# Kernel optimization log

Hardware: AMD Instinct MI355X
Metric: run time of the kernel (lower is better)

## Reference

```python
import jax, jax.numpy as jnp
import numpy as np

N = 10000          # nodes
E = 80000          # edges
STATE_DIM = 18
HID = 1024
LAYERS = 4


def setup_inputs() -> dict:
    key = jax.random.key(0)
    ks = jax.random.split(key, 16)
    s = 0.02
    x = jax.random.normal(ks[0], (N, STATE_DIM), dtype=jnp.float32)
    edge_index = jax.random.randint(ks[1], (2, E), 0, N, dtype=jnp.int32)
    # frozen inverse-phase embedding projection (no bias)
    proj_w = jax.random.normal(ks[2], (STATE_DIM, HID), dtype=jnp.float32) * s
    # per-layer message MLP: Linear(2*HID -> HID) -> ReLU -> Linear(HID -> HID)
    W1 = jax.random.normal(ks[3], (LAYERS, 2 * HID, HID), dtype=jnp.float32) * s
    b1 = jnp.zeros((LAYERS, HID), dtype=jnp.float32)
    W2 = jax.random.normal(ks[4], (LAYERS, HID, HID), dtype=jnp.float32) * s
    b2 = jnp.zeros((LAYERS, HID), dtype=jnp.float32)
    # ghost head: Linear(HID->256) -> ReLU -> Linear(256->1) -> Sigmoid
    gw1 = jax.random.normal(ks[5], (HID, 256), dtype=jnp.float32) * s
    gb1 = jnp.zeros((256,), dtype=jnp.float32)
    gw2 = jax.random.normal(ks[6], (256, 1), dtype=jnp.float32) * s
    gb2 = jnp.zeros((1,), dtype=jnp.float32)
    # state head: Linear(HID -> STATE_DIM)
    sw = jax.random.normal(ks[7], (HID, STATE_DIM), dtype=jnp.float32) * s
    sb = jnp.zeros((STATE_DIM,), dtype=jnp.float32)
    return {"x": x, "edge_index": edge_index, "proj_w": proj_w,
            "W1": W1, "b1": b1, "W2": W2, "b2": b2,
            "gw1": gw1, "gb1": gb1, "gw2": gw2, "gb2": gb2,
            "sw": sw, "sb": sb}


def reference(x, edge_index, proj_w, W1, b1, W2, b2, gw1, gb1, gw2, gb2, sw, sb):
    src = edge_index[0]  # j (source)
    dst = edge_index[1]  # i (target), aggr='add' scatters into i
    # InversePhaseEmbedding: sin(h)*cos(h)
    p = x @ proj_w                      # [N, HID]
    h = jnp.sin(p) * jnp.cos(p)
    for l in range(LAYERS):
        x_i = h[dst]                    # [E, HID] gather target feats
        x_j = h[src]                    # [E, HID] gather source feats
        msg = jnp.concatenate([x_i, x_j - x_i], axis=-1)  # [E, 2*HID]
        m = jax.nn.relu(msg @ W1[l] + b1[l]) @ W2[l] + b2[l]  # [E, HID]
        h = jax.ops.segment_sum(m, dst, num_segments=N)       # scatter-add
        h = jax.nn.relu(h)
    ghost_score = jax.nn.sigmoid(jax.nn.relu(h @ gw1 + gb1) @ gw2 + gb2)  # [N,1]
    stable_state = h @ sw + sb                                            # [N,18]
    return ghost_score, stable_state, h
```

## Files before the change

kernel.cpp:

```cpp
#include <hip/hip_runtime.h>
#include <hip/hip_bf16.h>
#include <math.h>

#define NN 10000
#define EE 80000
#define SDIM 18
#define HID 1024
#define NLAYERS 4
#define GHID 256

typedef __bf16 bf16;
typedef __bf16 bf16x8 __attribute__((ext_vector_type(8)));
typedef __bf16 bf16x4 __attribute__((ext_vector_type(4)));
typedef float f32x4 __attribute__((ext_vector_type(4)));

#define AS1C(p) ((const __attribute__((address_space(1))) void*)(p))
#define AS3(p)  ((__attribute__((address_space(3))) void*)(p))

__global__ void count_kernel(const int* __restrict__ ei, int* __restrict__ cnt) {
    int e = blockIdx.x * 256 + threadIdx.x;
    if (e < EE) atomicAdd(&cnt[ei[EE + e]], 1);
}

__global__ __launch_bounds__(256) void scan_kernel(const int* __restrict__ cnt,
                                                   int* __restrict__ offs,
                                                   int* __restrict__ cursor,
                                                   float* __restrict__ degF) {
    const int CH = 40;
    __shared__ int partial[256];
    int t = threadIdx.x;
    int base = t * CH;
    int local[CH];
    int sum = 0;
#pragma unroll
    for (int i = 0; i < CH; ++i) {
        int idx = base + i;
        int v = (idx < NN) ? cnt[idx] : 0;
        local[i] = sum;
        sum += v;
    }
    partial[t] = sum;
    __syncthreads();
    for (int off = 1; off < 256; off <<= 1) {
        int v = (t >= off) ? partial[t - off] : 0;
        __syncthreads();
        partial[t] += v;
        __syncthreads();
    }
    int excl = (t == 0) ? 0 : partial[t - 1];
#pragma unroll
    for (int i = 0; i < CH; ++i) {
        int idx = base + i;
        if (idx < NN) {
            int o = excl + local[i];
            offs[idx] = o;
            cursor[idx] = o;
            degF[idx] = (float)cnt[idx];
        }
    }
    if (t == 255) offs[NN] = partial[255];
}

__global__ void scatter_kernel(const int* __restrict__ ei, int* __restrict__ cursor,
                               int* __restrict__ esrc) {
    int e = blockIdx.x * 256 + threadIdx.x;
    if (e < EE) {
        int dst = ei[EE + e];
        int pos = atomicAdd(&cursor[dst], 1);
        esrc[pos] = ei[e];
    }
}

__global__ __launch_bounds__(256) void prep_kernel(const float* __restrict__ W1,
                                                   const float* __restrict__ W2,
                                                   const float* __restrict__ gw1,
                                                   const float* __restrict__ sw,
                                                   const float* __restrict__ b1,
                                                   bf16* __restrict__ WT,
                                                   bf16* __restrict__ W2t,
                                                   bf16* __restrict__ gw1t,
                                                   bf16* __restrict__ swt,
                                                   float* __restrict__ cb,
                                                   int* __restrict__ cnt) {
    __shared__ float td[32][33];
    __shared__ float tb[32][33];
    const size_t H2 = (size_t)HID * HID;
    int b = blockIdx.x;
    int tx = threadIdx.x & 31, ty = threadIdx.x >> 5;

    if (b < 4096) {
        int l = b >> 10, r = b & 1023;
        int bx = (r & 31) * 32, by = (r >> 5) * 32;
        const float* s = W1 + (size_t)l * 2 * H2;
        bf16* d = WT + (size_t)l * 2 * H2;
#pragma unroll
        for (int r4 = 0; r4 < 4; ++r4) {
            int row = by + ty + r4 * 8;
            float vt = s[(size_t)row * HID + bx + tx];
            float vb = s[H2 + (size_t)row * HID + bx + tx];
            td[ty + r4 * 8][tx] = vt - vb;
            tb[ty + r4 * 8][tx] = vb;
        }
        __syncthreads();
#pragma unroll
        for (int r4 = 0; r4 < 4; ++r4) {
            int orow = bx + ty + r4 * 8;
            d[(size_t)orow * HID + by + tx] = (bf16)td[tx][ty + r4 * 8];
            d[(size_t)(HID + orow) * HID + by + tx] = (bf16)tb[tx][ty + r4 * 8];
        }
    } else if (b < 8192) {
        int sub = b - 4096;
        int l = sub >> 10, r = sub & 1023;
        int bx = (r & 31) * 32, by = (r >> 5) * 32;
        const float* s = W2 + (size_t)l * H2;
        bf16* d = W2t + (size_t)l * H2;
#pragma unroll
        for (int r4 = 0; r4 < 4; ++r4) {
            int row = by + ty + r4 * 8;
            td[ty + r4 * 8][tx] = s[(size_t)row * HID + bx + tx];
        }
        __syncthreads();
#pragma unroll
        for (int r4 = 0; r4 < 4; ++r4) {
            int orow = bx + ty + r4 * 8;
            d[(size_t)orow * HID + by + tx] = (bf16)td[tx][ty + r4 * 8];
        }
    } else if (b < 8448) {
        int sub = b - 8192;
        int bx = (sub & 7) * 32, by = (sub >> 3) * 32;
#pragma unroll
        for (int r4 = 0; r4 < 4; ++r4) {
            int row = by + ty + r4 * 8;
            td[ty + r4 * 8][tx] = gw1[(size_t)row * GHID + bx + tx];
        }
        __syncthreads();
#pragma unroll
        for (int r4 = 0; r4 < 4; ++r4) {
            int orow = bx + ty + r4 * 8;
            gw1t[(size_t)orow * HID + by + tx] = (bf16)td[tx][ty + r4 * 8];
        }
    } else if (b < 8576) {
        int i = (b - 8448) * 256 + threadIdx.x;
        int n = i >> 10, k = i & 1023;
        swt[i] = (bf16)(n < SDIM ? sw[k * SDIM + n] : 0.f);
    } else if (b < 8608) {
        int i = (b - 8576) * 256 + threadIdx.x;
        int l = i >> 11, c = i & 2047;
        cb[i] = (c < HID) ? b1[l * HID + c] : 0.f;
    } else {
        int i = (b - 8608) * 256 + threadIdx.x;
        if (i < NN) cnt[i] = 0;
    }
}

__global__ __launch_bounds__(256) void proj_kernel(const float* __restrict__ x,
                                                   const float* __restrict__ pw,
                                                   bf16* __restrict__ hb) {
    int row = blockIdx.y;
    int col = blockIdx.x * 256 + threadIdx.x;
    __shared__ float xr[SDIM];
    if (threadIdx.x < SDIM) xr[threadIdx.x] = x[row * SDIM + threadIdx.x];
    __syncthreads();
    float acc = 0.f;
#pragma unroll
    for (int k = 0; k < SDIM; ++k) acc += xr[k] * pw[k * HID + col];
    hb[(size_t)row * HID + col] = (bf16)(sinf(acc) * cosf(acc));
}

template <int RELU, int HAS_BIAS, int HAS_RS, int WF32, int WB16>
__global__ __launch_bounds__(256) void mgemm_kernel(const bf16* __restrict__ A,
                                                    const bf16* __restrict__ Bt,
                                                    float* __restrict__ C,
                                                    bf16* __restrict__ Cb,
                                                    const float* __restrict__ bias,
                                                    const float* __restrict__ rowscale,
                                                    int M, int N, int K) {
    __shared__ bf16 As[2][128 * 32];
    __shared__ bf16 Bs[2][128 * 32];
    const int tid = threadIdx.x;

    const int num_n = gridDim.x, num_m = gridDim.y;
    int bid = blockIdx.x + blockIdx.y * num_n;
    const int GROUP = 8;
    int width = GROUP * num_n;
    int group = bid / width;
    int rem = bid - group * width;
    int rows_ing = num_m - group * GROUP;
    rows_ing = rows_ing < GROUP ? rows_ing : GROUP;
    int by = group * GROUP + rem % rows_ing;
    int bx = rem / rows_ing;
    const int m0 = by * 128;
    const int n0 = bx * 128;

    const int wave = tid >> 6;
    const int wr = (wave >> 1) * 64, wc = (wave & 1) * 64;
    const int lane = tid & 63;
    const int quad = lane >> 4, r15 = lane & 15;

    f32x4 acc[4][4] = {};

    const int s0 = tid, s1 = 256 + tid;
    int ar0 = m0 + (s0 >> 2); ar0 = ar0 < M ? ar0 : M - 1;
    int ar1 = m0 + (s1 >> 2); ar1 = ar1 < M ? ar1 : M - 1;
    const bf16* ga0 = A + (size_t)ar0 * K + (s0 & 3) * 8;
    const bf16* ga1 = A + (size_t)ar1 * K + (s1 & 3) * 8;
    const bf16* gb0 = Bt + (size_t)(n0 + (s0 >> 2)) * K + (s0 & 3) * 8;
    const bf16* gb1 = Bt + (size_t)(n0 + (s1 >> 2)) * K + (s1 & 3) * 8;
    const int lofs0 = (tid & ~63) * 8;
    const int lofs1 = 2048 + (tid & ~63) * 8;

    __builtin_amdgcn_global_load_lds(AS1C(ga0), AS3(&As[0][lofs0]), 16, 0, 0);
    __builtin_amdgcn_global_load_lds(AS1C(ga1), AS3(&As[0][lofs1]), 16, 0, 0);
    __builtin_amdgcn_global_load_lds(AS1C(gb0), AS3(&Bs[0][lofs0]), 16, 0, 0);
    __builtin_amdgcn_global_load_lds(AS1C(gb1), AS3(&Bs[0][lofs1]), 16, 0, 0);

    const int NIT = K >> 5;
    for (int k = 0; k < NIT; ++k) {
        const int buf = k & 1;
        __syncthreads();
        if (k + 1 < NIT) {
            const int ko = (k + 1) << 5;
            __builtin_amdgcn_global_load_lds(AS1C(ga0 + ko), AS3(&As[buf ^ 1][lofs0]), 16, 0, 0);
            __builtin_amdgcn_global_load_lds(AS1C(ga1 + ko), AS3(&As[buf ^ 1][lofs1]), 16, 0, 0);
            __builtin_amdgcn_global_load_lds(AS1C(gb0 + ko), AS3(&Bs[buf ^ 1][lofs0]), 16, 0, 0);
            __builtin_amdgcn_global_load_lds(AS1C(gb1 + ko), AS3(&Bs[buf ^ 1][lofs1]), 16, 0, 0);
        }
        bf16x8 af[4], bfr[4];
#pragma unroll
        for (int i = 0; i < 4; ++i)
            af[i] = *(const bf16x8*)(&As[buf][(wr + i * 16 + r15) * 32 + quad * 8]);
#pragma unroll
        for (int j = 0; j < 4; ++j)
            bfr[j] = *(const bf16x8*)(&Bs[buf][(wc + j * 16 + r15) * 32 + quad * 8]);
#pragma unroll
        for (int i = 0; i < 4; ++i)
#pragma unroll
            for (int j = 0; j < 4; ++j)
                acc[i][j] = __builtin_amdgcn_mfma_f32_16x16x32_bf16(af[i], bfr[j], acc[i][j], 0, 0, 0);
    }

#pragma unroll
    for (int i = 0; i < 4; ++i) {
#pragma unroll
        for (int r = 0; r < 4; ++r) {
            int grow = m0 + wr + i * 16 + quad * 4 + r;
            if (grow >= M) continue;
            float rs = HAS_RS ? rowscale[grow] : 1.f;
#pragma unroll
            for (int j = 0; j < 4; ++j) {
                int gcol = n0 + wc + j * 16 + r15;
                float v = acc[i][j][r];
                if (HAS_BIAS) v += rs * bias[gcol];
                if (RELU) v = fmaxf(v, 0.f);
                if (WF32) C[(size_t)grow * N + gcol] = v;
                if (WB16) Cb[(size_t)grow * N + gcol] = (bf16)v;
            }
        }
    }
}

__global__ __launch_bounds__(256) void gather_kernel(const int* __restrict__ offs,
                                                     const int* __restrict__ esrc,
                                                     const bf16* __restrict__ CB,
                                                     bf16* __restrict__ Sb) {
    int half = threadIdx.x >> 7;
    int t = threadIdx.x & 127;
    int node = blockIdx.x * 2 + half;
    int c = t * 8;
    int k0 = offs[node], k1 = offs[node + 1];
    bf16x8 cv = *(const bf16x8*)(CB + (size_t)node * 2048 + c);
    float cf[8], a[8];
#pragma unroll
    for (int i = 0; i < 8; ++i) { cf[i] = (float)cv[i]; a[i] = 0.f; }
    for (int k = k0; k < k1; ++k) {
        int s = esrc[k];
        bf16x8 bv = *(const bf16x8*)(CB + (size_t)s * 2048 + 1024 + c);
#pragma unroll
        for (int i = 0; i < 8; ++i) a[i] += fmaxf(cf[i] + (float)bv[i], 0.f);
    }
    bf16x8 o;
#pragma unroll
    for (int i = 0; i < 8; ++i) o[i] = (bf16)a[i];
    *(bf16x8*)(Sb + (size_t)node * HID + c) = o;
}

__global__ __launch_bounds__(64) void stable_mfma_kernel(const bf16* __restrict__ hb,
                                                         const bf16* __restrict__ swt,
                                                         const float* __restrict__ sb,
                                                         float* __restrict__ out) {
    int m0 = blockIdx.x * 16;
    int lane = threadIdx.x;
    int quad = lane >> 4, r15 = lane & 15;
    f32x4 acc0 = {}, acc1 = {};
    const bf16* arow = hb + (size_t)(m0 + r15) * HID + quad * 8;
    const bf16* b0 = swt + (size_t)r15 * HID + quad * 8;
    const bf16* b1p = swt + (size_t)(16 + r15) * HID + quad * 8;
    for (int k0 = 0; k0 < HID; k0 += 32) {
        bf16x8 af = *(const bf16x8*)(arow + k0);
        bf16x8 bf0 = *(const bf16x8*)(b0 + k0);
        bf16x8 bf1 = *(const bf16x8*)(b1p + k0);
        acc0 = __builtin_amdgcn_mfma_f32_16x16x32_bf16(af, bf0, acc0, 0, 0, 0);
        acc1 = __builtin_amdgcn_mfma_f32_16x16x32_bf16(af, bf1, acc1, 0, 0, 0);
    }
#pragma unroll
    for (int r = 0; r < 4; ++r) {
        int grow = m0 + quad * 4 + r;
        out[(size_t)grow * SDIM + r15] = acc0[r] + sb[r15];
        if (r15 < 2) out[(size_t)grow * SDIM + 16 + r15] = acc1[r] + sb[16 + r15];
    }
}

__global__ __launch_bounds__(256) void ghost_kernel(const float* __restrict__ g1,
                                                    const float* __restrict__ gw2,
                                                    const float* __restrict__ gb2,
                                                    float* __restrict__ out) {
    int w = threadIdx.x >> 6, lane = threadIdx.x & 63;
    int row = blockIdx.x * 4 + w;
    const float4 gv = *(const float4*)(g1 + (size_t)row * GHID + lane * 4);
    const float4 wv = *(const float4*)(gw2 + lane * 4);
    float v = gv.x * wv.x + gv.y * wv.y + gv.z * wv.z + gv.w * wv.w;
#pragma unroll
    for (int o = 32; o > 0; o >>= 1) v += __shfl_down(v, o, 64);
    if (lane == 0) out[row] = 1.f / (1.f + expf(-(v + gb2[0])));
}

extern "C" void kernel_launch(void* const* d_in, const int* in_sizes, int n_in,
                              void* d_out, int out_size, void* d_ws, size_t ws_size,
                              hipStream_t stream) {
    const float* x   = (const float*)d_in[0];
    const int*   ei  = (const int*)d_in[1];
    const float* pw  = (const float*)d_in[2];
    const float* W1  = (const float*)d_in[3];
    const float* b1  = (const float*)d_in[4];
    const float* W2  = (const float*)d_in[5];
    const float* b2  = (const float*)d_in[6];
    const float* gw1 = (const float*)d_in[7];
    const float* gb1 = (const float*)d_in[8];
    const float* gw2 = (const float*)d_in[9];
    const float* gb2 = (const float*)d_in[10];
    const float* sw  = (const float*)d_in[11];
    const float* sb  = (const float*)d_in[12];

    float* out    = (float*)d_out;
    float* ghost  = out;
    float* stable = out + NN;
    float* h      = out + NN + NN * SDIM;

    const size_t H2 = (size_t)HID * HID;
    float* ws   = (float*)d_ws;
    float* g1   = ws;
    float* degF = g1 + (size_t)NN * GHID;
    float* cb   = degF + NN;
    bf16* hb    = (bf16*)(cb + 4 * 2048);
    bf16* Sb    = hb + (size_t)NN * HID;
    bf16* CB    = Sb + (size_t)NN * HID;
    bf16* WT    = CB + (size_t)NN * 2048;
    bf16* W2t   = WT + 8 * H2;
    bf16* gw1t  = W2t + 4 * H2;
    bf16* swt   = gw1t + (size_t)GHID * HID;
    int*  cnt    = (int*)(swt + 32 * 1024);
    int*  offs   = cnt + NN;
    int*  cursor = offs + NN + 1;
    int*  esrc   = cursor + NN;

    prep_kernel<<<dim3(8648), 256, 0, stream>>>(W1, W2, gw1, sw, b1, WT, W2t, gw1t, swt, cb, cnt);

    count_kernel<<<dim3((EE + 255) / 256), 256, 0, stream>>>(ei, cnt);
    scan_kernel<<<dim3(1), 256, 0, stream>>>(cnt, offs, cursor, degF);
    scatter_kernel<<<dim3((EE + 255) / 256), 256, 0, stream>>>(ei, cursor, esrc);

    proj_kernel<<<dim3(HID / 256, NN), 256, 0, stream>>>(x, pw, hb);

    dim3 gfused(2048 / 128, (NN + 127) / 128);
    dim3 gw2g(HID / 128, (NN + 127) / 128);
    for (int l = 0; l < NLAYERS; ++l) {
        mgemm_kernel<0, 1, 0, 0, 1><<<gfused, 256, 0, stream>>>(
            hb, WT + (size_t)l * 2 * H2, nullptr, CB, cb + l * 2048, nullptr, NN, 2048, HID);
        gather_kernel<<<dim3(NN / 2), 256, 0, stream>>>(offs, esrc, CB, Sb);
        if (l < NLAYERS - 1)
            mgemm_kernel<1, 1, 1, 0, 1><<<gw2g, 256, 0, stream>>>(
                Sb, W2t + (size_t)l * H2, nullptr, hb, b2 + (size_t)l * HID, degF, NN, HID, HID);
        else
            mgemm_kernel<1, 1, 1, 1, 1><<<gw2g, 256, 0, stream>>>(
                Sb, W2t + (size_t)l * H2, h, hb, b2 + (size_t)l * HID, degF, NN, HID, HID);
    }

    mgemm_kernel<1, 1, 0, 1, 0><<<dim3(GHID / 128, (NN + 127) / 128), 256, 0, stream>>>(
        hb, gw1t, g1, nullptr, gb1, nullptr, NN, GHID, HID);
    ghost_kernel<<<dim3(NN / 4), 256, 0, stream>>>(g1, gw2, gb2, ghost);
    stable_mfma_kernel<<<dim3(NN / 16), 64, 0, stream>>>(hb, swt, sb, stable);
}
```

Baseline: 750.0 us.

## Add 256x256-tile 8-wave pipelined MFMA GEMM for layer GEMMs

Adds a new bf16 GEMM kernel with 256x256 output tiles, 512 threads, double-buffered direct global-to-LDS loads, swizzled LDS reads and interleaved barrier/priority scheduling. Both per-layer GEMMs (fused W1 and W2) now use it instead of the 128x128 kernel. Larger tiles raise arithmetic intensity and overlap loads with MFMA work. The cost is fewer blocks: the W2 GEMM gets only 4x40 tiles, which may underfill the GPU, and the 128KB LDS use limits occupancy.

```diff
diff --git a/kernel.cpp b/kernel.cpp
--- a/kernel.cpp
+++ b/kernel.cpp
@@ -257,6 +257,150 @@
             }
         }
     }
+}
+
+template <int RELU, int HAS_BIAS, int HAS_RS, int WF32, int WB16>
+__global__ __launch_bounds__(512, 2) void mgemm256_kernel(const bf16* __restrict__ A,
+                                                          const bf16* __restrict__ Bt,
+                                                          float* __restrict__ C,
+                                                          bf16* __restrict__ Cb,
+                                                          const float* __restrict__ bias,
+                                                          const float* __restrict__ rowscale,
+                                                          int M, int N, int K) {
+    __shared__ bf16 lds[65536];
+    const int tid = threadIdx.x;
+    const int wave = tid >> 6, lane = tid & 63;
+    const int wm = wave >> 2, wn = wave & 3;
+    const int quad = lane >> 4, r15 = lane & 15;
+    const int m0 = blockIdx.y * 256, n0 = blockIdx.x * 256;
+
+    const int srow = tid >> 3;
+    const int scol = ((tid & 7) ^ (srow & 7)) * 8;
+    const bf16* pa[4];
+    const bf16* pb[4];
+#pragma unroll
+    for (int v = 0; v < 4; ++v) {
+        int ra = m0 + v * 64 + srow;
+        ra = ra < M ? ra : M - 1;
+        pa[v] = A + (size_t)ra * K + scol;
+        pb[v] = Bt + (size_t)(n0 + v * 64 + srow) * K + scol;
+    }
+    const int ldst = (tid & ~63) * 8;
+
+    const int aBaseRd = r15 * 64;
+    const int bBaseRd = (wn & 1) * 4096 + r15 * 64;
+    const int sg0 = (quad ^ (r15 & 7)) * 8;
+    const int sg1 = sg0 ^ 32;
+
+#define STAGE_A(pi, h, kt)                                                                               \
+    do {                                                                                                 \
+        __builtin_amdgcn_global_load_lds(AS1C(pa[(h)*2 + 0] + (kt)*64),                                  \
+                                         AS3(&lds[((pi)*2 + (h)) * 8192 + ldst]), 16, 0, 0);             \
+        __builtin_amdgcn_global_load_lds(AS1C(pa[(h)*2 + 1] + (kt)*64),                                  \
+                                         AS3(&lds[((pi)*2 + (h)) * 8192 + 4096 + ldst]), 16, 0, 0);      \
+    } while (0)
+#define STAGE_B(pi, h, kt)                                                                               \
+    do {                                                                                                 \
+        __builtin_amdgcn_global_load_lds(AS1C(pb[(h)*2 + 0] + (kt)*64),                                  \
+                                         AS3(&lds[32768 + ((pi)*2 + (h)) * 8192 + ldst]), 16, 0, 0);     \
+        __builtin_amdgcn_global_load_lds(AS1C(pb[(h)*2 + 1] + (kt)*64),                                  \
+                                         AS3(&lds[32768 + ((pi)*2 + (h)) * 8192 + 4096 + ldst]), 16, 0, 0); \
+    } while (0)
+#define LD_A(pi, I)                                                                \
+    do {                                                                           \
+        _Pragma("unroll") for (int ii = 0; ii < 4; ++ii) {                         \
+            const bf16* p = &lds[((pi)*2 + wm) * 8192 + ((I) + ii) * 1024 + aBaseRd]; \
+            aF[ii * 2 + 0] = *(const bf16x8*)(p + sg0);                            \
+            aF[ii * 2 + 1] = *(const bf16x8*)(p + sg1);                            \
+        }                                                                          \
+    } while (0)
+#define LD_B(pi, J, dst)                                                           \
+    do {                                                                           \
+        _Pragma("unroll") for (int jj = 0; jj < 2; ++jj) {                         \
+            const bf16* p = &lds[32768 + ((pi)*2 + (wn >> 1)) * 8192 + bBaseRd + ((J) + jj) * 1024]; \
+            dst[jj * 2 + 0] = *(const bf16x8*)(p + sg0);                           \
+            dst[jj * 2 + 1] = *(const bf16x8*)(p + sg1);                           \
+        }                                                                          \
+    } while (0)
+#define MM(IB, JB, bsrc)                                                                                  \
+    do {                                                                                                  \
+        _Pragma("unroll") for (int ii = 0; ii < 4; ++ii)                                                  \
+            _Pragma("unroll") for (int jj = 0; jj < 2; ++jj)                                              \
+                _Pragma("unroll") for (int t = 0; t < 2; ++t)                                             \
+                    acc[(IB) + ii][(JB) + jj] = __builtin_amdgcn_mfma_f32_16x16x32_bf16(                  \
+                        aF[ii * 2 + t], bsrc[jj * 2 + t], acc[(IB) + ii][(JB) + jj], 0, 0, 0);            \
+    } while (0)
+#define BAR() __builtin_amdgcn_s_barrier()
+#define WLG() asm volatile("s_waitcnt lgkmcnt(0)")
+#define WVM4() asm volatile("s_waitcnt vmcnt(4)")
+#define PRIO(x) __builtin_amdgcn_s_setprio(x)
+
+    f32x4 acc[8][4] = {};
+    bf16x8 aF[8], bF0[4], bF1[4];
+
+    STAGE_B(0, 0, 0); STAGE_B(0, 1, 0);
+    STAGE_A(0, 0, 0); STAGE_A(0, 1, 0);
+    STAGE_B(1, 0, 1); STAGE_B(1, 1, 1);
+    WVM4();
+    BAR();
+
+    const int NT = K >> 6;
+    const int NI = NT >> 1;
+    for (int i = 0; i < NI; ++i) {
+        const int tO = 2 * i + 1;
+        int tE2 = 2 * i + 2; if (tE2 >= NT) tE2 -= 2;
+        int tO3 = 2 * i + 3; if (tO3 >= NT) tO3 -= 2;
+        LD_B(0, 0, bF0); LD_A(0, 0);
+        STAGE_A(1, 0, tO);
+        BAR(); WLG(); PRIO(1); MM(0, 0, bF0); PRIO(0); BAR();
+        LD_B(0, 2, bF1);
+        STAGE_A(1, 1, tO);
+        BAR(); WLG(); PRIO(1); MM(0, 2, bF1); PRIO(0); BAR();
+        LD_A(0, 4);
+        STAGE_B(0, 0, tE2);
+        BAR(); WLG(); PRIO(1); MM(4, 2, bF1); PRIO(0); BAR();
+        STAGE_B(0, 1, tE2);
+        BAR(); PRIO(1); MM(4, 0, bF0); PRIO(0); WVM4(); BAR();
+        LD_B(1, 0, bF0); LD_A(1, 0);
+        STAGE_A(0, 0, tE2);
+        BAR(); WLG(); PRIO(1); MM(0, 0, bF0); PRIO(0); BAR();
+        LD_B(1, 2, bF1);
+        STAGE_A(0, 1, tE2);
+        BAR(); WLG(); PRIO(1); MM(0, 2, bF1); PRIO(0); BAR();
+        LD_A(1, 4);
+        STAGE_B(1, 0, tO3);
+        BAR(); WLG(); PRIO(1); MM(4, 2, bF1); PRIO(0); BAR();
+        STAGE_B(1, 1, tO3);
+        BAR(); PRIO(1); MM(4, 0, bF0); PRIO(0); WVM4(); BAR();
+    }
+
+#pragma unroll
+    for (int i2 = 0; i2 < 8; ++i2) {
+#pragma unroll
+        for (int r = 0; r < 4; ++r) {
+            int grow = m0 + wm * 128 + i2 * 16 + quad * 4 + r;
+            if (grow >= M) continue;
+            float rs = HAS_RS ? rowscale[grow] : 1.f;
+#pragma unroll
+            for (int j = 0; j < 4; ++j) {
+                int gcol = n0 + wn * 64 + j * 16 + r15;
+                float v = acc[i2][j][r];
+                if (HAS_BIAS) v += rs * bias[gcol];
+                if (RELU) v = fmaxf(v, 0.f);
+                if (WF32) C[(size_t)grow * N + gcol] = v;
+                if (WB16) Cb[(size_t)grow * N + gcol] = (bf16)v;
+            }
+        }
+    }
+#undef STAGE_A
+#undef STAGE_B
+#undef LD_A
+#undef LD_B
+#undef MM
+#undef BAR
+#undef WLG
+#undef WVM4
+#undef PRIO
 }
 
 __global__ __launch_bounds__(256) void gather_kernel(const int* __restrict__ offs,
@@ -371,17 +515,17 @@
 
     proj_kernel<<<dim3(HID / 256, NN), 256, 0, stream>>>(x, pw, hb);
 
-    dim3 gfused(2048 / 128, (NN + 127) / 128);
-    dim3 gw2g(HID / 128, (NN + 127) / 128);
+    dim3 g256cb(2048 / 256, (NN + 255) / 256);
+    dim3 g256w2(HID / 256, (NN + 255) / 256);
     for (int l = 0; l < NLAYERS; ++l) {
-        mgemm_kernel<0, 1, 0, 0, 1><<<gfused, 256, 0, stream>>>(
+        mgemm256_kernel<0, 1, 0, 0, 1><<<g256cb, 512, 0, stream>>>(
             hb, WT + (size_t)l * 2 * H2, nullptr, CB, cb + l * 2048, nullptr, NN, 2048, HID);
         gather_kernel<<<dim3(NN / 2), 256, 0, stream>>>(offs, esrc, CB, Sb);
         if (l < NLAYERS - 1)
-            mgemm_kernel<1, 1, 1, 0, 1><<<gw2g, 256, 0, stream>>>(
+            mgemm256_kernel<1, 1, 1, 0, 1><<<g256w2, 512, 0, stream>>>(
                 Sb, W2t + (size_t)l * H2, nullptr, hb, b2 + (size_t)l * HID, degF, NN, HID, HID);
         else
-            mgemm_kernel<1, 1, 1, 1, 1><<<gw2g, 256, 0, stream>>>(
+            mgemm256_kernel<1, 1, 1, 1, 1><<<g256w2, 512, 0, stream>>>(
                 Sb, W2t + (size_t)l * H2, h, hb, b2 + (size_t)l * HID, degF, NN, HID, HID);
     }
 
```

Result: slower. 782.8 us (+4.4%).

## Add 256x128 triple-buffered MFMA GEMM kernel for per-layer node GEMMs

Applied to the files above, without the earlier changes.

Adds a new GEMM kernel with 512 threads and 256x128 output tiles. It stages A and B into LDS through global_load_lds with a triple-buffered K pipeline, XOR-swizzled LDS layout, s_setprio around the MFMA blocks, and a workgroup index remap to improve L2 locality. The per-layer fused W1 GEMM and the W2 GEMM now use it instead of the 128x128 kernel. The larger tiles raise data reuse and overlap loads with compute, but use 144 KB of LDS per block and leave fewer blocks in the grid, which may hurt occupancy and load balance.

```diff
diff --git a/kernel.cpp b/kernel.cpp
--- a/kernel.cpp
+++ b/kernel.cpp
@@ -257,6 +257,142 @@
             }
         }
     }
+}
+
+template <int RELU, int HAS_BIAS, int HAS_RS, int WF32, int WB16>
+__global__ __launch_bounds__(512, 2) void mgemm_big_kernel(const bf16* __restrict__ A,
+                                                           const bf16* __restrict__ Bt,
+                                                           float* __restrict__ C,
+                                                           bf16* __restrict__ Cb,
+                                                           const float* __restrict__ bias,
+                                                           const float* __restrict__ rowscale,
+                                                           int M, int N, int K) {
+    __shared__ bf16 lds[73728];
+    const int tid = threadIdx.x;
+    const int wave = tid >> 6, lane = tid & 63;
+    const int wm = wave >> 1, wn = wave & 1;
+    const int quad = lane >> 4, r15 = lane & 15;
+
+    const int nx = gridDim.x;
+    const int nwg = nx * gridDim.y;
+    const int bid = blockIdx.x + blockIdx.y * nx;
+    const int wg = (bid & 7) * (nwg >> 3) + (bid >> 3);
+    const int bx = wg % nx, by = wg / nx;
+    const int m0 = by * 256, n0 = bx * 128;
+
+    const int srow = tid >> 3;
+    const int scol = ((tid & 7) ^ (srow & 7)) * 8;
+    const bf16* pa[4];
+    const bf16* pb[2];
+#pragma unroll
+    for (int v = 0; v < 4; ++v) {
+        int ra = m0 + v * 64 + srow;
+        ra = ra < M ? ra : M - 1;
+        pa[v] = A + (size_t)ra * K + scol;
+    }
+#pragma unroll
+    for (int q = 0; q < 2; ++q)
+        pb[q] = Bt + (size_t)(n0 + q * 64 + srow) * K + scol;
+    const int ldst = (tid & ~63) * 8;
+
+    const int aHalf = wm >> 1;
+    const int aRowB = ((wm & 1) * 64 + r15) * 64;
+    const int bRowB = (wn * 64 + r15) * 64;
+    const int sg0 = (quad ^ (r15 & 7)) * 8;
+    const int sg1 = sg0 ^ 32;
+
+#define STAGE_A(b, h, kt)                                                                           \
+    do {                                                                                            \
+        __builtin_amdgcn_global_load_lds(AS1C(pa[(h)*2 + 0] + (kt)*64),                             \
+                                         AS3(&lds[((b)*2 + (h)) * 8192 + ldst]), 16, 0, 0);         \
+        __builtin_amdgcn_global_load_lds(AS1C(pa[(h)*2 + 1] + (kt)*64),                             \
+                                         AS3(&lds[((b)*2 + (h)) * 8192 + 4096 + ldst]), 16, 0, 0);  \
+    } while (0)
+#define STAGE_B(b, kt)                                                                              \
+    do {                                                                                            \
+        __builtin_amdgcn_global_load_lds(AS1C(pb[0] + (kt)*64),                                     \
+                                         AS3(&lds[49152 + (b)*8192 + ldst]), 16, 0, 0);             \
+        __builtin_amdgcn_global_load_lds(AS1C(pb[1] + (kt)*64),                                     \
+                                         AS3(&lds[49152 + (b)*8192 + 4096 + ldst]), 16, 0, 0);      \
+    } while (0)
+#define LD_A2(b, mfb)                                                              \
+    do {                                                                           \
+        _Pragma("unroll") for (int mi = 0; mi < 2; ++mi) {                         \
+            const bf16* p = &lds[((b)*2 + aHalf) * 8192 + aRowB + ((mfb) + mi) * 1024]; \
+            aF[mi * 2 + 0] = *(const bf16x8*)(p + sg0);                            \
+            aF[mi * 2 + 1] = *(const bf16x8*)(p + sg1);                            \
+        }                                                                          \
+    } while (0)
+#define LD_B8(b)                                                                   \
+    do {                                                                           \
+        _Pragma("unroll") for (int nf = 0; nf < 4; ++nf) {                         \
+            const bf16* p = &lds[49152 + (b)*8192 + bRowB + nf * 1024];            \
+            bF[nf * 2 + 0] = *(const bf16x8*)(p + sg0);                            \
+            bF[nf * 2 + 1] = *(const bf16x8*)(p + sg1);                            \
+        }                                                                          \
+    } while (0)
+#define MM2(mfb)                                                                                    \
+    do {                                                                                            \
+        _Pragma("unroll") for (int mi = 0; mi < 2; ++mi)                                            \
+            _Pragma("unroll") for (int nf = 0; nf < 4; ++nf)                                        \
+                _Pragma("unroll") for (int kh = 0; kh < 2; ++kh)                                    \
+                    acc[(mfb) + mi][nf] = __builtin_amdgcn_mfma_f32_16x16x32_bf16(                  \
+                        aF[mi * 2 + kh], bF[nf * 2 + kh], acc[(mfb) + mi][nf], 0, 0, 0);            \
+    } while (0)
+#define BAR() __builtin_amdgcn_s_barrier()
+#define WLG() asm volatile("s_waitcnt lgkmcnt(0)")
+#define WVM6() asm volatile("s_waitcnt vmcnt(6)")
+#define PRIO(x) __builtin_amdgcn_s_setprio(x)
+
+    f32x4 acc[4][4] = {};
+    bf16x8 aF[4], bF[8];
+
+    STAGE_A(0, 0, 0); STAGE_A(0, 1, 0); STAGE_B(0, 0);
+    STAGE_A(1, 0, 1); STAGE_A(1, 1, 1); STAGE_B(1, 1);
+    WVM6();
+    BAR();
+
+    const int NT = K >> 6;
+    int bt = 0, bs = 2;
+    for (int t = 0; t < NT; ++t) {
+        const int kt = (t + 2 < NT) ? (t + 2) : (t - 1);
+        LD_B8(bt); LD_A2(bt, 0);
+        STAGE_A(bs, 0, kt); STAGE_A(bs, 1, kt);
+        BAR(); WLG(); PRIO(1); MM2(0); PRIO(0); BAR();
+        LD_A2(bt, 2);
+        STAGE_B(bs, kt);
+        BAR(); WLG(); PRIO(1); MM2(2); PRIO(0); WVM6(); BAR();
+        bt = (bt == 2) ? 0 : bt + 1;
+        bs = (bs == 2) ? 0 : bs + 1;
+    }
+
+#pragma unroll
+    for (int mf = 0; mf < 4; ++mf) {
+#pragma unroll
+        for (int r = 0; r < 4; ++r) {
+            int grow = m0 + wm * 64 + mf * 16 + quad * 4 + r;
+            if (grow >= M) continue;
+            float rs = HAS_RS ? rowscale[grow] : 1.f;
+#pragma unroll
+            for (int nf = 0; nf < 4; ++nf) {
+                int gcol = n0 + wn * 64 + nf * 16 + r15;
+                float v = acc[mf][nf][r];
+                if (HAS_BIAS) v += rs * bias[gcol];
+                if (RELU) v = fmaxf(v, 0.f);
+                if (WF32) C[(size_t)grow * N + gcol] = v;
+                if (WB16) Cb[(size_t)grow * N + gcol] = (bf16)v;
+            }
+        }
+    }
+#undef STAGE_A
+#undef STAGE_B
+#undef LD_A2
+#undef LD_B8
+#undef MM2
+#undef BAR
+#undef WLG
+#undef WVM6
+#undef PRIO
 }
 
 __global__ __launch_bounds__(256) void gather_kernel(const int* __restrict__ offs,
@@ -371,17 +507,17 @@
 
     proj_kernel<<<dim3(HID / 256, NN), 256, 0, stream>>>(x, pw, hb);
 
-    dim3 gfused(2048 / 128, (NN + 127) / 128);
-    dim3 gw2g(HID / 128, (NN + 127) / 128);
+    dim3 gbigcb(2048 / 128, (NN + 255) / 256);
+    dim3 gbigw2(HID / 128, (NN + 255) / 256);
     for (int l = 0; l < NLAYERS; ++l) {
-        mgemm_kernel<0, 1, 0, 0, 1><<<gfused, 256, 0, stream>>>(
+        mgemm_big_kernel<0, 1, 0, 0, 1><<<gbigcb, 512, 0, stream>>>(
             hb, WT + (size_t)l * 2 * H2, nullptr, CB, cb + l * 2048, nullptr, NN, 2048, HID);
         gather_kernel<<<dim3(NN / 2), 256, 0, stream>>>(offs, esrc, CB, Sb);
         if (l < NLAYERS - 1)
-            mgemm_kernel<1, 1, 1, 0, 1><<<gw2g, 256, 0, stream>>>(
+            mgemm_big_kernel<1, 1, 1, 0, 1><<<gbigw2, 512, 0, stream>>>(
                 Sb, W2t + (size_t)l * H2, nullptr, hb, b2 + (size_t)l * HID, degF, NN, HID, HID);
         else
-            mgemm_kernel<1, 1, 1, 1, 1><<<gw2g, 256, 0, stream>>>(
+            mgemm_big_kernel<1, 1, 1, 1, 1><<<gbigw2, 512, 0, stream>>>(
                 Sb, W2t + (size_t)l * H2, h, hb, b2 + (size_t)l * HID, degF, NN, HID, HID);
     }
 
```

Measured after the change: 812.3 us. 1.08x slower.

## Triple-buffer GEMM LDS pipeline with swizzled layout and one barrier per tile

Applied to the files above, without the earlier changes.

Replaces the double-buffered bf16 MFMA GEMM with a three-stage LDS ring. Global-to-LDS loads for tile t+2 are issued while tile t is computed, with partial vmcnt waits and a single barrier per k-step. An XOR swizzle on the 16-byte segments is meant to avoid LDS bank conflicts on fragment reads, and MFMA sections run at raised wave priority. The launch bound requests 3 blocks per CU. LDS use grows to 48KB per block, which may limit occupancy, and the redundant reload on tail iterations adds some extra traffic.

```diff
diff --git a/kernel.cpp b/kernel.cpp
--- a/kernel.cpp
+++ b/kernel.cpp
@@ -168,16 +168,18 @@
 }
 
 template <int RELU, int HAS_BIAS, int HAS_RS, int WF32, int WB16>
-__global__ __launch_bounds__(256) void mgemm_kernel(const bf16* __restrict__ A,
-                                                    const bf16* __restrict__ Bt,
-                                                    float* __restrict__ C,
-                                                    bf16* __restrict__ Cb,
-                                                    const float* __restrict__ bias,
-                                                    const float* __restrict__ rowscale,
-                                                    int M, int N, int K) {
-    __shared__ bf16 As[2][128 * 32];
-    __shared__ bf16 Bs[2][128 * 32];
+__global__ __launch_bounds__(256, 3) void mgemm3_kernel(const bf16* __restrict__ A,
+                                                        const bf16* __restrict__ Bt,
+                                                        float* __restrict__ C,
+                                                        bf16* __restrict__ Cb,
+                                                        const float* __restrict__ bias,
+                                                        const float* __restrict__ rowscale,
+                                                        int M, int N, int K) {
+    __shared__ bf16 lds[24576];
     const int tid = threadIdx.x;
+    const int wave = tid >> 6, lane = tid & 63;
+    const int wm = wave >> 1, wn = wave & 1;
+    const int quad = lane >> 4, r15 = lane & 15;
 
     const int num_n = gridDim.x, num_m = gridDim.y;
     int bid = blockIdx.x + blockIdx.y * num_n;
@@ -189,66 +191,82 @@
     rows_ing = rows_ing < GROUP ? rows_ing : GROUP;
     int by = group * GROUP + rem % rows_ing;
     int bx = rem / rows_ing;
-    const int m0 = by * 128;
-    const int n0 = bx * 128;
-
-    const int wave = tid >> 6;
-    const int wr = (wave >> 1) * 64, wc = (wave & 1) * 64;
-    const int lane = tid & 63;
-    const int quad = lane >> 4, r15 = lane & 15;
+    const int m0 = by * 128, n0 = bx * 128;
+
+    const int strow = tid >> 2;
+    const int segsw = ((tid & 3) ^ ((tid >> 3) & 3)) * 8;
+    int ar0 = m0 + strow;       ar0 = ar0 < M ? ar0 : M - 1;
+    int ar1 = m0 + 64 + strow;  ar1 = ar1 < M ? ar1 : M - 1;
+    const bf16* ga0 = A + (size_t)ar0 * K + segsw;
+    const bf16* ga1 = A + (size_t)ar1 * K + segsw;
+    const bf16* gb0 = Bt + (size_t)(n0 + strow) * K + segsw;
+    const bf16* gb1 = Bt + (size_t)(n0 + 64 + strow) * K + segsw;
+    const int ldst = (tid & ~63) * 8;
+
+    int aoff[4], boff[4];
+#pragma unroll
+    for (int i = 0; i < 4; ++i) {
+        int rA = wm * 64 + i * 16 + r15;
+        aoff[i] = 12288 + rA * 32 + (quad ^ ((rA >> 1) & 3)) * 8;
+        int rB = wn * 64 + i * 16 + r15;
+        boff[i] = rB * 32 + (quad ^ ((rB >> 1) & 3)) * 8;
+    }
 
     f32x4 acc[4][4] = {};
 
-    const int s0 = tid, s1 = 256 + tid;
-    int ar0 = m0 + (s0 >> 2); ar0 = ar0 < M ? ar0 : M - 1;
-    int ar1 = m0 + (s1 >> 2); ar1 = ar1 < M ? ar1 : M - 1;
-    const bf16* ga0 = A + (size_t)ar0 * K + (s0 & 3) * 8;
-    const bf16* ga1 = A + (size_t)ar1 * K + (s1 & 3) * 8;
-    const bf16* gb0 = Bt + (size_t)(n0 + (s0 >> 2)) * K + (s0 & 3) * 8;
-    const bf16* gb1 = Bt + (size_t)(n0 + (s1 >> 2)) * K + (s1 & 3) * 8;
-    const int lofs0 = (tid & ~63) * 8;
-    const int lofs1 = 2048 + (tid & ~63) * 8;
-
-    __builtin_amdgcn_global_load_lds(AS1C(ga0), AS3(&As[0][lofs0]), 16, 0, 0);
-    __builtin_amdgcn_global_load_lds(AS1C(ga1), AS3(&As[0][lofs1]), 16, 0, 0);
-    __builtin_amdgcn_global_load_lds(AS1C(gb0), AS3(&Bs[0][lofs0]), 16, 0, 0);
-    __builtin_amdgcn_global_load_lds(AS1C(gb1), AS3(&Bs[0][lofs1]), 16, 0, 0);
-
-    const int NIT = K >> 5;
-    for (int k = 0; k < NIT; ++k) {
-        const int buf = k & 1;
-        __syncthreads();
-        if (k + 1 < NIT) {
-            const int ko = (k + 1) << 5;
-            __builtin_amdgcn_global_load_lds(AS1C(ga0 + ko), AS3(&As[buf ^ 1][lofs0]), 16, 0, 0);
-            __builtin_amdgcn_global_load_lds(AS1C(ga1 + ko), AS3(&As[buf ^ 1][lofs1]), 16, 0, 0);
-            __builtin_amdgcn_global_load_lds(AS1C(gb0 + ko), AS3(&Bs[buf ^ 1][lofs0]), 16, 0, 0);
-            __builtin_amdgcn_global_load_lds(AS1C(gb1 + ko), AS3(&Bs[buf ^ 1][lofs1]), 16, 0, 0);
-        }
-        bf16x8 af[4], bfr[4];
-#pragma unroll
-        for (int i = 0; i < 4; ++i)
-            af[i] = *(const bf16x8*)(&As[buf][(wr + i * 16 + r15) * 32 + quad * 8]);
-#pragma unroll
-        for (int j = 0; j < 4; ++j)
-            bfr[j] = *(const bf16x8*)(&Bs[buf][(wc + j * 16 + r15) * 32 + quad * 8]);
-#pragma unroll
-        for (int i = 0; i < 4; ++i)
-#pragma unroll
-            for (int j = 0; j < 4; ++j)
-                acc[i][j] = __builtin_amdgcn_mfma_f32_16x16x32_bf16(af[i], bfr[j], acc[i][j], 0, 0, 0);
-    }
+#define STAGE3(bs, kt)                                                                                   \
+    do {                                                                                                 \
+        const int ko_ = (kt) << 5;                                                                       \
+        __builtin_amdgcn_global_load_lds(AS1C(ga0 + ko_), AS3(&lds[12288 + (bs)*4096 + ldst]), 16, 0, 0); \
+        __builtin_amdgcn_global_load_lds(AS1C(ga1 + ko_), AS3(&lds[12288 + (bs)*4096 + 2048 + ldst]), 16, 0, 0); \
+        __builtin_amdgcn_global_load_lds(AS1C(gb0 + ko_), AS3(&lds[(bs)*4096 + ldst]), 16, 0, 0);        \
+        __builtin_amdgcn_global_load_lds(AS1C(gb1 + ko_), AS3(&lds[(bs)*4096 + 2048 + ldst]), 16, 0, 0); \
+    } while (0)
+
+    STAGE3(0, 0);
+    STAGE3(1, 1);
+    asm volatile("s_waitcnt vmcnt(4)");
+    __builtin_amdgcn_s_barrier();
+
+    const int NT = K >> 5;
+    int t = 0;
+
+#define TILE3(bi, bs)                                                                          \
+    do {                                                                                       \
+        int kt = (t + 2 < NT) ? (t + 2) : (t - 1);  \
+        bf16x8 aF[4], bF[4];                                                                   \
+        _Pragma("unroll") for (int i = 0; i < 4; ++i)                                          \
+            aF[i] = *(const bf16x8*)(&lds[(bi)*4096 + aoff[i]]);                               \
+        _Pragma("unroll") for (int j = 0; j < 4; ++j)                                          \
+            bF[j] = *(const bf16x8*)(&lds[(bi)*4096 + boff[j]]);                               \
+        STAGE3(bs, kt);                                                                        \
+        asm volatile("s_waitcnt lgkmcnt(0)");                                                  \
+        __builtin_amdgcn_s_setprio(1);                                                         \
+        _Pragma("unroll") for (int i = 0; i < 4; ++i)                                          \
+            _Pragma("unroll") for (int j = 0; j < 4; ++j)                                      \
+                acc[i][j] = __builtin_amdgcn_mfma_f32_16x16x32_bf16(aF[i], bF[j], acc[i][j], 0, 0, 0); \
+        __builtin_amdgcn_s_setprio(0);                                                         \
+        asm volatile("s_waitcnt vmcnt(4)");          \
+        __builtin_amdgcn_s_barrier();                                                          \
+        ++t;                                                                                   \
+    } while (0)
+
+    while (t + 3 <= NT) { TILE3(0, 2); TILE3(1, 0); TILE3(2, 1); }
+    if (t < NT) TILE3(0, 2);
+    if (t < NT) TILE3(1, 0);
+#undef TILE3
+#undef STAGE3
 
 #pragma unroll
     for (int i = 0; i < 4; ++i) {
 #pragma unroll
         for (int r = 0; r < 4; ++r) {
-            int grow = m0 + wr + i * 16 + quad * 4 + r;
+            int grow = m0 + wm * 64 + i * 16 + quad * 4 + r;
             if (grow >= M) continue;
             float rs = HAS_RS ? rowscale[grow] : 1.f;
 #pragma unroll
             for (int j = 0; j < 4; ++j) {
-                int gcol = n0 + wc + j * 16 + r15;
+                int gcol = n0 + wn * 64 + j * 16 + r15;
                 float v = acc[i][j][r];
                 if (HAS_BIAS) v += rs * bias[gcol];
                 if (RELU) v = fmaxf(v, 0.f);
@@ -371,21 +389,21 @@
 
     proj_kernel<<<dim3(HID / 256, NN), 256, 0, stream>>>(x, pw, hb);
 
-    dim3 gfused(2048 / 128, (NN + 127) / 128);
-    dim3 gw2g(HID / 128, (NN + 127) / 128);
+    dim3 gcbg(2048 / 128, (NN + 127) / 128);
+    dim3 gw2grid(HID / 128, (NN + 127) / 128);
     for (int l = 0; l < NLAYERS; ++l) {
-        mgemm_kernel<0, 1, 0, 0, 1><<<gfused, 256, 0, stream>>>(
+        mgemm3_kernel<0, 1, 0, 0, 1><<<gcbg, 256, 0, stream>>>(
             hb, WT + (size_t)l * 2 * H2, nullptr, CB, cb + l * 2048, nullptr, NN, 2048, HID);
         gather_kernel<<<dim3(NN / 2), 256, 0, stream>>>(offs, esrc, CB, Sb);
         if (l < NLAYERS - 1)
-            mgemm_kernel<1, 1, 1, 0, 1><<<gw2g, 256, 0, stream>>>(
+            mgemm3_kernel<1, 1, 1, 0, 1><<<gw2grid, 256, 0, stream>>>(
                 Sb, W2t + (size_t)l * H2, nullptr, hb, b2 + (size_t)l * HID, degF, NN, HID, HID);
         else
-            mgemm_kernel<1, 1, 1, 1, 1><<<gw2g, 256, 0, stream>>>(
+            mgemm3_kernel<1, 1, 1, 1, 1><<<gw2grid, 256, 0, stream>>>(
                 Sb, W2t + (size_t)l * H2, h, hb, b2 + (size_t)l * HID, degF, NN, HID, HID);
     }
 
-    mgemm_kernel<1, 1, 0, 1, 0><<<dim3(GHID / 128, (NN + 127) / 128), 256, 0, stream>>>(
+    mgemm3_kernel<1, 1, 0, 1, 0><<<dim3(GHID / 128, (NN + 127) / 128), 256, 0, stream>>>(
         hb, gw1t, g1, nullptr, gb1, nullptr, NN, GHID, HID);
     ghost_kernel<<<dim3(NN / 4), 256, 0, stream>>>(g1, gw2, gb2, ghost);
     stable_mfma_kernel<<<dim3(NN / 16), 64, 0, stream>>>(hb, swt, sb, stable);
```

Measured after the change: 716.1 us. -4.5%, faster.
